# Kernel tuning notes

Measured on AMD Instinct MI355X. Metric: run time of the kernel, lower is better.

The kernel has to match this reference:

```python
import jax, jax.numpy as jnp
import numpy as np

N_FREQS = 8
ALPHA = 16.0
SCALING = ALPHA / N_FREQS  # alpha / n_freqs
EPS = 1e-8


def setup_inputs() -> dict:
    key = jax.random.key(0)
    ks = jax.random.split(key, 6)
    B, S, IN, OUT = 4, 2048, 4096, 4096
    x = jax.random.normal(ks[0], (B, S, IN), dtype=jnp.float32)
    W = jax.random.normal(ks[1], (OUT, IN), dtype=jnp.float32) * 0.02
    bias = jax.random.normal(ks[2], (OUT,), dtype=jnp.float32) * 0.02
    delta_real = jax.random.normal(ks[3], (N_FREQS, N_FREQS), dtype=jnp.float32)
    delta_imag = jax.random.normal(ks[4], (N_FREQS, N_FREQS), dtype=jnp.float32)
    # m is initialized in torch as row-norm of the base weight; emulate that here
    m = jnp.linalg.norm(W, axis=1, keepdims=True)
    return {"x": x, "W": W, "bias": bias,
            "delta_real": delta_real, "delta_imag": delta_imag, "m": m}


def _dora_weight(W, delta_real, delta_imag, m):
    # full-size rfft2 of the frozen base weight (norm='ortho')
    W_fft = jnp.fft.rfft2(W, norm="ortho")            # [OUT, IN//2+1] complex
    fh, fw = delta_real.shape                          # freq_h, freq_w (low-freq corner)
    delta = jax.lax.complex(delta_real, delta_imag) * SCALING
    W_fft = W_fft.at[:fh, :fw].add(delta)              # pad-to-full + add, fused
    W_mod = jnp.fft.irfft2(W_fft, s=W.shape, norm="ortho")  # [OUT, IN] real
    # DoRA: magnitude m times unit row-direction
    norm = jnp.linalg.norm(W_mod, axis=1, keepdims=True)     # [OUT, 1]
    return m * W_mod / (norm + EPS)


def reference(x, W, bias, delta_real, delta_imag, m):
    W_dora = _dora_weight(W, delta_real, delta_imag, m)      # [OUT, IN]
    # F.linear: x @ W^T + b
    return jnp.einsum("bsi,oi->bso", x, W_dora) + bias
```

## Files before the change

### kernel.cpp

```cpp
#include <hip/hip_runtime.h>
#include <hip/hip_bf16.h>

typedef __attribute__((ext_vector_type(4))) float f32x4;
typedef __attribute__((ext_vector_type(8))) short bf16x8;

#define IN_DIM 4096
#define OUT_DIM 4096
#define MROWS 8192
#define NFREQ 8
#define TWO_PI 6.283185307179586f

#define BK 64
#define NT (IN_DIM / BK)
#define LDS_BUF 32768
#define LDS_HALF 16384
#define LDS_B_REGION 65536

__device__ __forceinline__ unsigned int f2bf(float f) {
    union { float f; unsigned int u; } a;
    a.f = f;
    unsigned int u = a.u;
    u += 0x7fffu + ((u >> 16) & 1u);
    return u >> 16;
}

__global__ __launch_bounds__(256) void dora_weight_kernel(
    const float* __restrict__ W,
    const float* __restrict__ dre,
    const float* __restrict__ dimg,
    const float* __restrict__ mrow,
    unsigned short* __restrict__ Wd)
{
    const int o = blockIdx.x;
    const int t = threadIdx.x;

    float P[NFREQ], Q[NFREQ];
#pragma unroll
    for (int w = 0; w < NFREQ; ++w) { P[w] = 0.f; Q[w] = 0.f; }
#pragma unroll
    for (int h = 0; h < NFREQ; ++h) {
        const float th = (TWO_PI / 4096.0f) * (float)((h * o) & 4095);
        float sh, ch;
        sincosf(th, &sh, &ch);
#pragma unroll
        for (int w = 0; w < NFREQ; ++w) {
            const float A = 2.0f * dre[h * NFREQ + w];
            const float B = 2.0f * dimg[h * NFREQ + w];
            P[w] += A * ch - B * sh;
            Q[w] += A * sh + B * ch;
        }
    }
#pragma unroll
    for (int w = 0; w < NFREQ; ++w) {
        const float c = (w == 0 ? 1.0f : 2.0f) * (1.0f / 4096.0f);
        P[w] *= c; Q[w] *= c;
    }

    const int i0 = t * 16;
    const f32x4* wrow = (const f32x4*)(W + (size_t)o * IN_DIM + i0);
    float vals[16];
    float ss = 0.0f;
#pragma unroll
    for (int q = 0; q < 4; ++q) {
        const f32x4 wv = wrow[q];
#pragma unroll
        for (int j = 0; j < 4; ++j) {
            const int i = i0 + q * 4 + j;
            const float beta = (TWO_PI / 4096.0f) * (float)i;
            float sb, cb;
            sincosf(beta, &sb, &cb);
            float cw = cb, sw = sb;
            float d = P[0] + P[1] * cw - Q[1] * sw;
#pragma unroll
            for (int w = 2; w < NFREQ; ++w) {
                const float cn = cw * cb - sw * sb;
                sw = sw * cb + cw * sb;
                cw = cn;
                d += P[w] * cw - Q[w] * sw;
            }
            const float v = wv[j] + d;
            vals[q * 4 + j] = v;
            ss += v * v;
        }
    }

#pragma unroll
    for (int off = 32; off > 0; off >>= 1)
        ss += __shfl_down(ss, off, 64);
    __shared__ float red[4];
    if ((t & 63) == 0) red[t >> 6] = ss;
    __syncthreads();
    const float n2 = red[0] + red[1] + red[2] + red[3];
    const float scale = mrow[o] / (sqrtf(n2) + 1e-8f);

    unsigned int wds[8];
#pragma unroll
    for (int k = 0; k < 8; ++k)
        wds[k] = f2bf(vals[2 * k] * scale) | (f2bf(vals[2 * k + 1] * scale) << 16);
    uint4* dst = (uint4*)(Wd + (size_t)o * IN_DIM + i0);
    dst[0] = make_uint4(wds[0], wds[1], wds[2], wds[3]);
    dst[1] = make_uint4(wds[4], wds[5], wds[6], wds[7]);
}

__global__ __launch_bounds__(256) void cvt_kernel(
    const float* __restrict__ x, unsigned short* __restrict__ xb)
{
    const size_t idx = (size_t)blockIdx.x * 256 + threadIdx.x;
    const f32x4* p = (const f32x4*)(x + idx * 8);
    const f32x4 a = p[0], b = p[1];
    uint4 o;
    o.x = f2bf(a[0]) | (f2bf(a[1]) << 16);
    o.y = f2bf(a[2]) | (f2bf(a[3]) << 16);
    o.z = f2bf(b[0]) | (f2bf(b[1]) << 16);
    o.w = f2bf(b[2]) | (f2bf(b[3]) << 16);
    *(uint4*)(xb + idx * 8) = o;
}


#define GLOAD(src, ldsoff)                                                    \
    __builtin_amdgcn_global_load_lds(                                         \
        (const __attribute__((address_space(1))) void*)(src),                 \
        (__attribute__((address_space(3))) void*)(smem + (ldsoff)), 16, 0, 0)

#define SBAR      asm volatile("s_barrier" ::: "memory")
#define WAITLGKM  asm volatile("s_waitcnt lgkmcnt(0)" ::: "memory")

__device__ __forceinline__ void mfma16(
    f32x4 (&acc)[8][4], const bf16x8 (&af)[4][2], const bf16x8 (&bf)[2][2],
    int MH, int NH)
{
#pragma unroll
    for (int ks = 0; ks < 2; ++ks)
#pragma unroll
        for (int mf = 0; mf < 4; ++mf)
#pragma unroll
            for (int nf = 0; nf < 2; ++nf)
                acc[MH * 4 + mf][NH * 2 + nf] =
                    __builtin_amdgcn_mfma_f32_16x16x32_bf16(
                        af[mf][ks], bf[nf][ks], acc[MH * 4 + mf][NH * 2 + nf],
                        0, 0, 0);
}

__global__ __launch_bounds__(512, 2) void gemm8_kernel(
    const unsigned short* __restrict__ Xb,
    const unsigned short* __restrict__ Wd,
    const float* __restrict__ bias,
    float* __restrict__ out)
{
    __shared__ __align__(1024) unsigned char smem[131072];

    const int tid = threadIdx.x;
    const int wid = tid >> 6, lane = tid & 63;
    const int wr = wid >> 2, wc = wid & 3;
    const int fr = lane & 15, fq = lane >> 4;

    const int bid = blockIdx.x;
    const int lin = (bid & 7) * 64 + (bid >> 3);
    const int tm = lin & 31, tn = lin >> 5;
    const int m0 = tm * 256, n0 = tn * 256;

    const int srr = wid * 16 + (lane >> 3);
    const int scc = ((lane & 7) ^ (lane >> 3)) * 8;
    const unsigned short* aS = Xb + (size_t)(m0 + srr) * IN_DIM + scc;
    const unsigned short* bS = Wd + (size_t)(n0 + srr) * IN_DIM + scc;
    const int sdst = wid * 2048;

    const int cbyte = ((fq ^ (fr & 7)) * 16);
    const int aBase0 = (wr * 128 + fr) * 128 + cbyte;
    const int aBase1 = aBase0 ^ 64;
    const int bBase0 = LDS_B_REGION + (wc * 64 + fr) * 128 + cbyte;
    const int bBase1 = bBase0 ^ 64;

    auto STAGE = [&](int buf, int isB, int half, int tt) {
        const unsigned short* s =
            (isB ? bS : aS) + (size_t)half * 128 * IN_DIM + (size_t)tt * BK;
        const int d = buf * LDS_BUF + isB * LDS_B_REGION + half * LDS_HALF + sdst;
        GLOAD(s, d);
        GLOAD(s + 8 * IN_DIM, d + 1024);
    };

    f32x4 acc[8][4] = {};
    bf16x8 a0[4][2], a1[4][2], bb[2][2];

    STAGE(0, 0, 0, 0); STAGE(0, 0, 1, 0);
    STAGE(0, 1, 0, 0); STAGE(0, 1, 1, 0);
    STAGE(1, 0, 0, 1); STAGE(1, 0, 1, 1);
    asm volatile("s_waitcnt vmcnt(4)" ::: "memory");
    SBAR;

    for (int t = 0; t < NT; ++t) {
        const int b = t & 1;
        const int bo = b * LDS_BUF;
        const bool st1 = (t + 1 < NT);
        const bool st2 = (t + 2 < NT);

#pragma unroll
        for (int mf = 0; mf < 4; ++mf) {
            a0[mf][0] = *(const bf16x8*)(smem + bo + aBase0 + mf * 2048);
            a0[mf][1] = *(const bf16x8*)(smem + bo + aBase1 + mf * 2048);
        }
#pragma unroll
        for (int nf = 0; nf < 2; ++nf) {
            bb[nf][0] = *(const bf16x8*)(smem + bo + bBase0 + nf * 2048);
            bb[nf][1] = *(const bf16x8*)(smem + bo + bBase1 + nf * 2048);
        }
        if (st1) STAGE(b ^ 1, 1, 0, t + 1);
        SBAR;
        WAITLGKM;
        __builtin_amdgcn_s_setprio(1);
        mfma16(acc, a0, bb, 0, 0);
        __builtin_amdgcn_s_setprio(0);
        SBAR;

#pragma unroll
        for (int mf = 0; mf < 4; ++mf) {
            a1[mf][0] = *(const bf16x8*)(smem + bo + aBase0 + 8192 + mf * 2048);
            a1[mf][1] = *(const bf16x8*)(smem + bo + aBase1 + 8192 + mf * 2048);
        }
        if (st1) STAGE(b ^ 1, 1, 1, t + 1);
        SBAR;
        WAITLGKM;
        __builtin_amdgcn_s_setprio(1);
        mfma16(acc, a1, bb, 1, 0);
        __builtin_amdgcn_s_setprio(0);
        SBAR;

#pragma unroll
        for (int nf = 0; nf < 2; ++nf) {
            bb[nf][0] = *(const bf16x8*)(smem + bo + bBase0 + 4096 + nf * 2048);
            bb[nf][1] = *(const bf16x8*)(smem + bo + bBase1 + 4096 + nf * 2048);
        }
        if (st2) STAGE(b, 0, 0, t + 2);
        SBAR;
        WAITLGKM;
        __builtin_amdgcn_s_setprio(1);
        mfma16(acc, a1, bb, 1, 1);
        __builtin_amdgcn_s_setprio(0);
        SBAR;

        if (st2) STAGE(b, 0, 1, t + 2);
        SBAR;
        WAITLGKM;
        __builtin_amdgcn_s_setprio(1);
        mfma16(acc, a0, bb, 0, 1);
        __builtin_amdgcn_s_setprio(0);
        if (st2) {
            asm volatile("s_waitcnt vmcnt(4)" ::: "memory");
        } else {
            asm volatile("s_waitcnt vmcnt(0)" ::: "memory");
        }
        SBAR;
    }

#pragma unroll
    for (int nf = 0; nf < 4; ++nf) {
        const int col = n0 + wc * 64 + nf * 16 + fr;
        const float bv = bias[col];
#pragma unroll
        for (int mf = 0; mf < 8; ++mf) {
            const int row = m0 + wr * 128 + mf * 16 + fq * 4;
            float* op = out + (size_t)row * OUT_DIM + col;
            op[0 * OUT_DIM] = acc[mf][nf][0] + bv;
            op[1 * OUT_DIM] = acc[mf][nf][1] + bv;
            op[2 * OUT_DIM] = acc[mf][nf][2] + bv;
            op[3 * OUT_DIM] = acc[mf][nf][3] + bv;
        }
    }
}

__global__ __launch_bounds__(256) void gemm_fallback(
    const float* __restrict__ Xf,
    const unsigned short* __restrict__ Wd,
    const float* __restrict__ bias,
    float* __restrict__ out)
{
    __shared__ unsigned short As[2][128 * 32];
    __shared__ unsigned short Bs[2][128 * 32];

    const int t = threadIdx.x;
    const int wid = t >> 6, lane = t & 63;
    const int wr = wid >> 1, wc = wid & 1;
    const int m0 = blockIdx.x * 128, n0 = blockIdx.y * 128;
    const int fr = lane & 15, fq = lane >> 4;

    f32x4 acc[4][4] = {};

    const int srow = wid * 16 + (lane >> 2);
    const int scol = (lane & 3) * 8;
    const unsigned short* bsrc0 = Wd + (size_t)(n0 + srow) * IN_DIM + scol;
    const unsigned short* bsrc1 = bsrc0 + (size_t)64 * IN_DIM;
    const int lds_off = wid * 512;

    const int ar = t >> 1;
    const int ak = (t & 1) * 16;
    const float* afp = Xf + (size_t)(m0 + ar) * IN_DIM + ak;
    const int a_lds_off = ar * 32 + ak;

    auto stageB = [&](unsigned short* ldsbase, int kt) {
        __builtin_amdgcn_global_load_lds(
            (const __attribute__((address_space(1))) void*)(bsrc0 + kt * 32),
            (__attribute__((address_space(3))) void*)(ldsbase + lds_off), 16, 0, 0);
        __builtin_amdgcn_global_load_lds(
            (const __attribute__((address_space(1))) void*)(bsrc1 + kt * 32),
            (__attribute__((address_space(3))) void*)(ldsbase + 2048 + lds_off), 16, 0, 0);
    };
    auto writeA = [&](int buf, const f32x4* v) {
        unsigned int w[8];
#pragma unroll
        for (int k = 0; k < 4; ++k) {
            w[2 * k]     = f2bf(v[k][0]) | (f2bf(v[k][1]) << 16);
            w[2 * k + 1] = f2bf(v[k][2]) | (f2bf(v[k][3]) << 16);
        }
        uint4* d = (uint4*)(&As[buf][a_lds_off]);
        d[0] = make_uint4(w[0], w[1], w[2], w[3]);
        d[1] = make_uint4(w[4], w[5], w[6], w[7]);
    };

    stageB(Bs[0], 0);
    {
        f32x4 av[4];
        const f32x4* ap = (const f32x4*)afp;
        av[0] = ap[0]; av[1] = ap[1]; av[2] = ap[2]; av[3] = ap[3];
        writeA(0, av);
    }
    __syncthreads();

    for (int kt = 0; kt < IN_DIM / 32; ++kt) {
        const int cur = kt & 1;
        const bool more = (kt + 1 < IN_DIM / 32);
        f32x4 nv[4];
        if (more) {
            const f32x4* ap = (const f32x4*)(afp + (size_t)(kt + 1) * 32);
            nv[0] = ap[0]; nv[1] = ap[1]; nv[2] = ap[2]; nv[3] = ap[3];
            stageB(Bs[cur ^ 1], kt + 1);
        }
        bf16x8 afrag[4], bfrag[4];
#pragma unroll
        for (int mf = 0; mf < 4; ++mf)
            afrag[mf] = *(const bf16x8*)(&As[cur][(wr * 64 + mf * 16 + fr) * 32 + fq * 8]);
#pragma unroll
        for (int nf = 0; nf < 4; ++nf)
            bfrag[nf] = *(const bf16x8*)(&Bs[cur][(wc * 64 + nf * 16 + fr) * 32 + fq * 8]);
#pragma unroll
        for (int mf = 0; mf < 4; ++mf)
#pragma unroll
            for (int nf = 0; nf < 4; ++nf)
                acc[mf][nf] = __builtin_amdgcn_mfma_f32_16x16x32_bf16(
                    afrag[mf], bfrag[nf], acc[mf][nf], 0, 0, 0);
        if (more) writeA(cur ^ 1, nv);
        __syncthreads();
    }

#pragma unroll
    for (int nf = 0; nf < 4; ++nf) {
        const int col = n0 + wc * 64 + nf * 16 + fr;
        const float bv = bias[col];
#pragma unroll
        for (int mf = 0; mf < 4; ++mf) {
            const int row = m0 + wr * 64 + mf * 16 + fq * 4;
            float* op = out + (size_t)row * OUT_DIM + col;
            op[0 * OUT_DIM] = acc[mf][nf][0] + bv;
            op[1 * OUT_DIM] = acc[mf][nf][1] + bv;
            op[2 * OUT_DIM] = acc[mf][nf][2] + bv;
            op[3 * OUT_DIM] = acc[mf][nf][3] + bv;
        }
    }
}

extern "C" void kernel_launch(void* const* d_in, const int* in_sizes, int n_in,
                              void* d_out, int out_size, void* d_ws, size_t ws_size,
                              hipStream_t stream) {
    const float* x    = (const float*)d_in[0];
    const float* W    = (const float*)d_in[1];
    const float* bias = (const float*)d_in[2];
    const float* dre  = (const float*)d_in[3];
    const float* dimg = (const float*)d_in[4];
    const float* mrow = (const float*)d_in[5];
    float* out = (float*)d_out;

    unsigned short* Wd = (unsigned short*)d_ws;
    const size_t WD_BYTES = (size_t)OUT_DIM * IN_DIM * 2;
    const size_t XB_BYTES = (size_t)MROWS * IN_DIM * 2;
    unsigned short* Xb = (unsigned short*)((char*)d_ws + WD_BYTES);
    const bool fast = ws_size >= WD_BYTES + XB_BYTES;

    dora_weight_kernel<<<OUT_DIM, 256, 0, stream>>>(W, dre, dimg, mrow, Wd);

    if (fast) {
        cvt_kernel<<<(MROWS * (size_t)IN_DIM / 8) / 256, 256, 0, stream>>>(x, Xb);
        gemm8_kernel<<<dim3((MROWS / 256) * (OUT_DIM / 256)), dim3(512), 0, stream>>>(
            Xb, Wd, bias, out);
    } else {
        dim3 grid(MROWS / 128, OUT_DIM / 128);
        gemm_fallback<<<grid, dim3(256), 0, stream>>>(x, Wd, bias, out);
    }
}
```

Before: 331.7 us.

## Fuse prep kernels, use fast trig recurrence, and relax GEMM barriers

Merges the DoRA weight kernel and the x-to-bf16 conversion into one launch. It replaces per-element sincosf with __sinf/__cosf plus an incremental rotation recurrence, and restructures the GEMM main loop. In the GEMM, B-tile staging moves one stage earlier, most intra-iteration barriers and lgkmcnt waits are dropped, and launch bounds change to one block per CU. Dropping the barriers could open LDS read/write races, and the fast trig functions add small numerical error.

```diff
diff --git a/kernel.cpp b/kernel.cpp
--- a/kernel.cpp
+++ b/kernel.cpp
@@ -24,15 +24,34 @@
     return u >> 16;
 }
 
-__global__ __launch_bounds__(256) void dora_weight_kernel(
+#define ROT_C 0.9999988234517019f
+#define ROT_S 0.0015339801862847655f
+
+__global__ __launch_bounds__(256) void prep_kernel(
+    const float* __restrict__ x,
     const float* __restrict__ W,
     const float* __restrict__ dre,
     const float* __restrict__ dimg,
     const float* __restrict__ mrow,
-    unsigned short* __restrict__ Wd)
+    unsigned short* __restrict__ Wd,
+    unsigned short* __restrict__ xb)
 {
+    const int t = threadIdx.x;
+
+    if (blockIdx.x >= OUT_DIM) {
+        const size_t idx = (size_t)(blockIdx.x - OUT_DIM) * 256 + t;
+        const f32x4* p = (const f32x4*)(x + idx * 8);
+        const f32x4 a = p[0], b = p[1];
+        uint4 o;
+        o.x = f2bf(a[0]) | (f2bf(a[1]) << 16);
+        o.y = f2bf(a[2]) | (f2bf(a[3]) << 16);
+        o.z = f2bf(b[0]) | (f2bf(b[1]) << 16);
+        o.w = f2bf(b[2]) | (f2bf(b[3]) << 16);
+        *(uint4*)(xb + idx * 8) = o;
+        return;
+    }
+
     const int o = blockIdx.x;
-    const int t = threadIdx.x;
 
     float P[NFREQ], Q[NFREQ];
 #pragma unroll
@@ -40,8 +59,7 @@
 #pragma unroll
     for (int h = 0; h < NFREQ; ++h) {
         const float th = (TWO_PI / 4096.0f) * (float)((h * o) & 4095);
-        float sh, ch;
-        sincosf(th, &sh, &ch);
+        const float sh = __sinf(th), ch = __cosf(th);
 #pragma unroll
         for (int w = 0; w < NFREQ; ++w) {
             const float A = 2.0f * dre[h * NFREQ + w];
@@ -60,15 +78,15 @@
     const f32x4* wrow = (const f32x4*)(W + (size_t)o * IN_DIM + i0);
     float vals[16];
     float ss = 0.0f;
+
+    const float beta0 = (TWO_PI / 4096.0f) * (float)i0;
+    float cb = __cosf(beta0), sb = __sinf(beta0);
+
 #pragma unroll
     for (int q = 0; q < 4; ++q) {
         const f32x4 wv = wrow[q];
 #pragma unroll
         for (int j = 0; j < 4; ++j) {
-            const int i = i0 + q * 4 + j;
-            const float beta = (TWO_PI / 4096.0f) * (float)i;
-            float sb, cb;
-            sincosf(beta, &sb, &cb);
             float cw = cb, sw = sb;
             float d = P[0] + P[1] * cw - Q[1] * sw;
 #pragma unroll
@@ -81,6 +99,9 @@
             const float v = wv[j] + d;
             vals[q * 4 + j] = v;
             ss += v * v;
+            const float cbn = cb * ROT_C - sb * ROT_S;
+            sb = sb * ROT_C + cb * ROT_S;
+            cb = cbn;
         }
     }
 
@@ -102,28 +123,13 @@
     dst[1] = make_uint4(wds[4], wds[5], wds[6], wds[7]);
 }
 
-__global__ __launch_bounds__(256) void cvt_kernel(
-    const float* __restrict__ x, unsigned short* __restrict__ xb)
-{
-    const size_t idx = (size_t)blockIdx.x * 256 + threadIdx.x;
-    const f32x4* p = (const f32x4*)(x + idx * 8);
-    const f32x4 a = p[0], b = p[1];
-    uint4 o;
-    o.x = f2bf(a[0]) | (f2bf(a[1]) << 16);
-    o.y = f2bf(a[2]) | (f2bf(a[3]) << 16);
-    o.z = f2bf(b[0]) | (f2bf(b[1]) << 16);
-    o.w = f2bf(b[2]) | (f2bf(b[3]) << 16);
-    *(uint4*)(xb + idx * 8) = o;
-}
-
 
 #define GLOAD(src, ldsoff)                                                    \
     __builtin_amdgcn_global_load_lds(                                         \
         (const __attribute__((address_space(1))) void*)(src),                 \
         (__attribute__((address_space(3))) void*)(smem + (ldsoff)), 16, 0, 0)
 
-#define SBAR      asm volatile("s_barrier" ::: "memory")
-#define WAITLGKM  asm volatile("s_waitcnt lgkmcnt(0)" ::: "memory")
+#define SBAR asm volatile("s_barrier" ::: "memory")
 
 __device__ __forceinline__ void mfma16(
     f32x4 (&acc)[8][4], const bf16x8 (&af)[4][2], const bf16x8 (&bf)[2][2],
@@ -141,7 +147,7 @@
                         0, 0, 0);
 }
 
-__global__ __launch_bounds__(512, 2) void gemm8_kernel(
+__global__ __launch_bounds__(512, 1) void gemm8_kernel(
     const unsigned short* __restrict__ Xb,
     const unsigned short* __restrict__ Wd,
     const float* __restrict__ bias,
@@ -185,7 +191,8 @@
     STAGE(0, 0, 0, 0); STAGE(0, 0, 1, 0);
     STAGE(0, 1, 0, 0); STAGE(0, 1, 1, 0);
     STAGE(1, 0, 0, 1); STAGE(1, 0, 1, 1);
-    asm volatile("s_waitcnt vmcnt(4)" ::: "memory");
+    STAGE(1, 1, 0, 1);
+    asm volatile("s_waitcnt vmcnt(6)" ::: "memory");
     SBAR;
 
     for (int t = 0; t < NT; ++t) {
@@ -204,22 +211,16 @@
             bb[nf][0] = *(const bf16x8*)(smem + bo + bBase0 + nf * 2048);
             bb[nf][1] = *(const bf16x8*)(smem + bo + bBase1 + nf * 2048);
         }
-        if (st1) STAGE(b ^ 1, 1, 0, t + 1);
-        SBAR;
-        WAITLGKM;
+        if (st1) STAGE(b ^ 1, 1, 1, t + 1);
         __builtin_amdgcn_s_setprio(1);
         mfma16(acc, a0, bb, 0, 0);
         __builtin_amdgcn_s_setprio(0);
-        SBAR;
 
 #pragma unroll
         for (int mf = 0; mf < 4; ++mf) {
             a1[mf][0] = *(const bf16x8*)(smem + bo + aBase0 + 8192 + mf * 2048);
             a1[mf][1] = *(const bf16x8*)(smem + bo + aBase1 + 8192 + mf * 2048);
         }
-        if (st1) STAGE(b ^ 1, 1, 1, t + 1);
-        SBAR;
-        WAITLGKM;
         __builtin_amdgcn_s_setprio(1);
         mfma16(acc, a1, bb, 1, 0);
         __builtin_amdgcn_s_setprio(0);
@@ -231,21 +232,17 @@
             bb[nf][1] = *(const bf16x8*)(smem + bo + bBase1 + 4096 + nf * 2048);
         }
         if (st2) STAGE(b, 0, 0, t + 2);
-        SBAR;
-        WAITLGKM;
         __builtin_amdgcn_s_setprio(1);
         mfma16(acc, a1, bb, 1, 1);
         __builtin_amdgcn_s_setprio(0);
         SBAR;
 
-        if (st2) STAGE(b, 0, 1, t + 2);
-        SBAR;
-        WAITLGKM;
+        if (st2) { STAGE(b, 0, 1, t + 2); STAGE(b, 1, 0, t + 2); }
         __builtin_amdgcn_s_setprio(1);
         mfma16(acc, a0, bb, 0, 1);
         __builtin_amdgcn_s_setprio(0);
         if (st2) {
-            asm volatile("s_waitcnt vmcnt(4)" ::: "memory");
+            asm volatile("s_waitcnt vmcnt(6)" ::: "memory");
         } else {
             asm volatile("s_waitcnt vmcnt(0)" ::: "memory");
         }
@@ -384,13 +381,14 @@
     unsigned short* Xb = (unsigned short*)((char*)d_ws + WD_BYTES);
     const bool fast = ws_size >= WD_BYTES + XB_BYTES;
 
-    dora_weight_kernel<<<OUT_DIM, 256, 0, stream>>>(W, dre, dimg, mrow, Wd);
-
     if (fast) {
-        cvt_kernel<<<(MROWS * (size_t)IN_DIM / 8) / 256, 256, 0, stream>>>(x, Xb);
+        const int cvt_blocks = (MROWS * (size_t)IN_DIM / 8) / 256;
+        prep_kernel<<<OUT_DIM + cvt_blocks, 256, 0, stream>>>(
+            x, W, dre, dimg, mrow, Wd, Xb);
         gemm8_kernel<<<dim3((MROWS / 256) * (OUT_DIM / 256)), dim3(512), 0, stream>>>(
             Xb, Wd, bias, out);
     } else {
+        prep_kernel<<<OUT_DIM, 256, 0, stream>>>(x, W, dre, dimg, mrow, Wd, Wd);
         dim3 grid(MROWS / 128, OUT_DIM / 128);
         gemm_fallback<<<grid, dim3(256), 0, stream>>>(x, Wd, bias, out);
     }
```

Result: faster. 310.3 us (-6.4%).
